# Optimization experiments

Hardware: AMD Instinct MI355X
Metric: run time of the kernel (lower is better)

The kernel has to match this reference:

```python
import jax, jax.numpy as jnp
import numpy as np

N_NODES = 50000
N_EDGES = 800000
HIDDEN = 128
HEADS = 8
HEAD_DIM = HIDDEN // HEADS
N_LAYERS = 2
BATCH = 64
INPUT = 300


def setup_inputs() -> dict:
    key = jax.random.key(0)
    ks = jax.random.split(key, 10)
    s = 0.05
    word_embed_matrix = jax.random.normal(ks[0], (N_NODES, INPUT), dtype=jnp.float32)
    edge_index = jax.random.randint(ks[1], (2, N_EDGES), 0, N_NODES, dtype=jnp.int32)
    target_idx = jax.random.randint(ks[2], (BATCH,), 0, N_NODES, dtype=jnp.int32)
    # labels: first half positive, second half negative (batch/2 pos as in original loss)
    label_id = jnp.concatenate([jnp.ones(BATCH // 2, jnp.int32), jnp.zeros(BATCH // 2, jnp.int32)])
    lin1_W = jax.random.normal(ks[3], (INPUT, HIDDEN), dtype=jnp.float32) * s
    lin1_b = jnp.zeros((HIDDEN,), jnp.float32)
    gat_W = jax.random.normal(ks[4], (N_LAYERS, HIDDEN, HIDDEN), dtype=jnp.float32) * s
    gat_att_src = jax.random.normal(ks[5], (N_LAYERS, HEADS, HEAD_DIM), dtype=jnp.float32) * s
    gat_att_dst = jax.random.normal(ks[6], (N_LAYERS, HEADS, HEAD_DIM), dtype=jnp.float32) * s
    gat_bias = jnp.zeros((N_LAYERS, HIDDEN), jnp.float32)
    lin3_W = jax.random.normal(ks[7], (HIDDEN, 1), dtype=jnp.float32) * s
    lin3_b = jnp.zeros((1,), jnp.float32)
    return {"word_embed_matrix": word_embed_matrix, "edge_index": edge_index,
            "target_idx": target_idx, "label_id": label_id,
            "lin1_W": lin1_W, "lin1_b": lin1_b, "gat_W": gat_W,
            "gat_att_src": gat_att_src, "gat_att_dst": gat_att_dst,
            "gat_bias": gat_bias, "lin3_W": lin3_W, "lin3_b": lin3_b}


def gat_layer(x, src, dst, W, a_src, a_dst, b):
    # x: [N, HIDDEN]; src/dst: [E'] (self loops included)
    N = x.shape[0]
    h = (x @ W).reshape(N, HEADS, HEAD_DIM)               # [N,H,C]
    alpha_src = jnp.sum(h * a_src, axis=-1)               # [N,H]
    alpha_dst = jnp.sum(h * a_dst, axis=-1)               # [N,H]
    e = jax.nn.leaky_relu(alpha_src[src] + alpha_dst[dst], 0.2)  # [E',H]
    # softmax over incoming edges of each dst node (segment softmax)
    emax = jax.ops.segment_max(e, dst, num_segments=N)    # [N,H]
    ee = jnp.exp(e - emax[dst])
    denom = jax.ops.segment_sum(ee, dst, num_segments=N)  # [N,H]
    alpha = ee / denom[dst]                               # [E',H]
    msg = h[src] * alpha[:, :, None]                      # [E',H,C]
    out = jax.ops.segment_sum(msg, dst, num_segments=N)   # [N,H,C]
    return out.reshape(N, HIDDEN) + b


def reference(word_embed_matrix, edge_index, target_idx, label_id,
              lin1_W, lin1_b, gat_W, gat_att_src, gat_att_dst, gat_bias,
              lin3_W, lin3_b):
    N = word_embed_matrix.shape[0]
    # add self loops (PyG GATConv default)
    loop = jnp.arange(N, dtype=edge_index.dtype)
    src = jnp.concatenate([edge_index[0], loop])
    dst = jnp.concatenate([edge_index[1], loop])
    x = word_embed_matrix @ lin1_W + lin1_b
    for i in range(N_LAYERS):
        x = jax.nn.elu(gat_layer(x, src, dst, gat_W[i], gat_att_src[i], gat_att_dst[i], gat_bias[i]))
    target_embed = x[target_idx]                          # [B, HIDDEN]
    total_score = (target_embed @ lin3_W + lin3_b)[:, 0]  # [B]
    # labels are [1]*B/2 + [0]*B/2 (static layout, matches label_id)
    half = BATCH // 2
    pos_score = total_score[:half]
    neg_score = total_score[half:]
    loss = jnp.mean(jax.nn.relu(1.0 - (pos_score - neg_score)))
    return (total_score, loss)
```

## Files before the change

kernel.cpp:

```cpp
#include <hip/hip_runtime.h>
#include <math.h>

#define N_NODES 50000
#define N_EDGESI 800000
#define E_TOT   850000
#define HIDDEN  128
#define HEADS   8
#define HEAD_DIM 16
#define INPUT   300
#define BATCH   64

#define NR    128
#define RSZ   391
#define CAP   8192
#define CHUNK 2048
#define NSB   ((E_TOT + CHUNK - 1)/CHUNK)

typedef __bf16 bf16_t;
typedef bf16_t bf16x8 __attribute__((ext_vector_type(8)));
typedef bf16_t bf16x2 __attribute__((ext_vector_type(2)));
typedef float  f32x4  __attribute__((ext_vector_type(4)));
typedef float  f32x2  __attribute__((ext_vector_type(2)));

__global__ void wa_kernel(const float* __restrict__ W, const float* __restrict__ as,
                          const float* __restrict__ ad, float* __restrict__ Wa){
    int k = threadIdx.x;
    #pragma unroll
    for (int j = 0; j < 8; j++){
        float s1 = 0.f, s2 = 0.f;
        #pragma unroll
        for (int d = 0; d < 16; d++){
            float wv = W[k*128 + j*16 + d];
            s1 += wv * as[j*16 + d];
            s2 += wv * ad[j*16 + d];
        }
        Wa[k*16 + j]     = s1;
        Wa[k*16 + 8 + j] = s2;
    }
}

template<int K_REAL, int K_PAD, int NCOL>
__global__ void fused_pack_kernel(const float* __restrict__ W1, const float* __restrict__ Wg,
                                  const float* __restrict__ Wa, const float* __restrict__ b1,
                                  bf16_t* __restrict__ bF, float* __restrict__ bcomb){
    int idx = blockIdx.x*256 + threadIdx.x;
    if (idx < NCOL){
        float s = 0.f;
        for (int d = 0; d < 128; d++)
            s += b1[d] * ((idx < 128) ? Wg[d*128 + idx] : Wa[d*16 + (idx - 128)]);
        bcomb[idx] = s;
    }
    if (idx >= K_PAD*NCOL) return;
    int k = idx / NCOL, col = idx % NCOL;
    float v = 0.f;
    if (k < K_REAL){
        const float* w1r = W1 + k*128;
        if (col < 128){
            for (int m = 0; m < 128; m++) v += w1r[m] * Wg[m*128 + col];
        } else {
            int jj = col - 128;
            for (int m = 0; m < 128; m++) v += w1r[m] * Wa[m*16 + jj];
        }
    }
    int o = ((k >> 3)*NCOL + col)*8 + (k & 7);
    bF[o] = (bf16_t)v;
}

template<int K_REAL, int K_PAD, int NCOL, bool ALPHA>
__global__ void pack_b_kernel(const float* __restrict__ B128, const float* __restrict__ as,
                              const float* __restrict__ ad, bf16_t* __restrict__ bHi){
    int idx = blockIdx.x*256 + threadIdx.x;
    if (idx >= K_PAD*NCOL) return;
    int k = idx / NCOL, col = idx % NCOL;
    float v = 0.f;
    if (k < K_REAL){
        if (!ALPHA || col < 128){
            v = B128[k*128 + col];
        } else {
            int jj = col - 128;
            const float* a = (jj < 8) ? (as + jj*16) : (ad + (jj-8)*16);
            const float* wrow = B128 + k*128 + (jj & 7)*16;
            float s = 0.f;
            #pragma unroll
            for (int d = 0; d < 16; d++) s += wrow[d]*a[d];
            v = s;
        }
    }
    int o = ((k >> 3)*NCOL + col)*8 + (k & 7);
    bHi[o] = (bf16_t)v;
}

template<int K_REAL, int K_PAD, int NT, int GH, int PD, bool A_BF16, bool BIAS_EPI, bool ALPHA, bool OUT8>
__global__ __launch_bounds__(256)
void mfma_gemm6_kernel(const void* __restrict__ A_, const bf16_t* __restrict__ bHi,
                       const float* __restrict__ bias, void* __restrict__ outP,
                       float* __restrict__ asrc_out, float* __restrict__ adst_out, int M)
{
    constexpr int NCOL   = NT * 16;
    constexpr int KSTEPS = K_PAD / 32;
    constexpr int KSPP   = GH / 4;
    constexpr int NPASS  = KSTEPS / KSPP;
    constexpr int PELEM  = GH * NCOL * 8;
    constexpr int SIT    = PELEM / 2048;
    static_assert(KSPP * NPASS == KSTEPS && SIT * 2048 == PELEM, "");
    __shared__ bf16_t blds[PELEM];

    int tid = threadIdx.x, lane = tid & 63, w = tid >> 6;
    int l15 = lane & 15, lg = lane >> 4;
    int m0 = (blockIdx.x*4 + w) * 16;
    int mrow = m0 + l15; if (mrow >= M) mrow = M - 1;

    const float*  arowF = (const float*) A_ + (size_t)mrow*K_REAL;
    const bf16_t* arowB = (const bf16_t*)A_ + (size_t)mrow*K_REAL;

    float4 pva[PD], pvb[PD];
    bf16x8 pab[PD];
    #pragma unroll
    for (int i = 0; i < PD; i++){
        int k0 = i*32 + lg*8;
        if (A_BF16){
            pab[i] = *(const bf16x8*)&arowB[k0];
        } else {
            pva[i] = (k0 + 3 < K_REAL) ? *(const float4*)&arowF[k0]     : (float4){0.f,0.f,0.f,0.f};
            pvb[i] = (k0 + 7 < K_REAL) ? *(const float4*)&arowF[k0 + 4] : (float4){0.f,0.f,0.f,0.f};
        }
    }

    f32x4 acc[NT];
    #pragma unroll
    for (int c = 0; c < NT; c++) acc[c] = (f32x4){0.f,0.f,0.f,0.f};

    #pragma unroll
    for (int p = 0; p < NPASS; p++){
        const bf16_t* gB = bHi + (size_t)p*PELEM;
        if (p) __syncthreads();
        #pragma unroll
        for (int it = 0; it < SIT; it++){
            int idx = (tid + it*256)*8;
            *(bf16x8*)&blds[idx] = *(const bf16x8*)&gB[idx];
        }
        __syncthreads();

        #pragma unroll
        for (int i = 0; i < KSPP; i++){
            const int ks = p*KSPP + i;
            const int sl = ks % PD;
            bf16x8 ah;
            if (A_BF16){
                ah = pab[sl];
            } else {
                float4 va = pva[sl], vb = pvb[sl];
                float f[8] = {va.x, va.y, va.z, va.w, vb.x, vb.y, vb.z, vb.w};
                #pragma unroll
                for (int q = 0; q < 8; q++) ah[q] = (bf16_t)f[q];
            }
            if (ks + PD < KSTEPS){
                int k0 = (ks + PD)*32 + lg*8;
                if (A_BF16){
                    pab[sl] = *(const bf16x8*)&arowB[k0];
                } else {
                    pva[sl] = (k0 + 3 < K_REAL) ? *(const float4*)&arowF[k0]     : (float4){0.f,0.f,0.f,0.f};
                    pvb[sl] = (k0 + 7 < K_REAL) ? *(const float4*)&arowF[k0 + 4] : (float4){0.f,0.f,0.f,0.f};
                }
            }
            int gloc = i*4 + lg;
            const bf16_t* b_base = &blds[(gloc*NCOL + l15)*8];
            #pragma unroll
            for (int c = 0; c < NT; c++){
                bf16x8 bh = *(const bf16x8*)&b_base[c*128];
                acc[c] = __builtin_amdgcn_mfma_f32_16x16x32_bf16(ah, bh, acc[c], 0,0,0);
            }
        }
    }

    #pragma unroll
    for (int c = 0; c < 8; c++){
        int col = c*16 + l15;
        float bv = BIAS_EPI ? bias[col] : 0.f;
        #pragma unroll
        for (int r = 0; r < 4; r++){
            int m = m0 + lg*4 + r;
            if (m < M){
                float v = acc[c][r] + bv;
                if (OUT8){
                    int pk = __builtin_amdgcn_cvt_pk_fp8_f32(v, v, 0, false);
                    ((unsigned char*)outP)[(size_t)m*128 + col] = (unsigned char)(pk & 0xff);
                } else {
                    ((bf16_t*)outP)[(size_t)m*128 + col] = (bf16_t)v;
                }
            }
        }
    }
    if (ALPHA){
        float bv8 = BIAS_EPI ? bias[128 + l15] : 0.f;
        #pragma unroll
        for (int r = 0; r < 4; r++){
            int m = m0 + lg*4 + r;
            if (m < M){
                float v = acc[8][r] + bv8;
                if (l15 < 8) asrc_out[m*8 + l15]       = v;
                else         adst_out[m*8 + (l15 - 8)] = v;
            }
        }
    }
}

__global__ void zero_cnt_kernel(int* __restrict__ bucket_cnt){
    bucket_cnt[threadIdx.x] = 0;
}

__global__ __launch_bounds__(256)
void block_sort_kernel(const int* __restrict__ ei, int* __restrict__ bucket_cnt,
                       int2* __restrict__ pairs2){
    __shared__ int2 stageL[CHUNK];
    __shared__ int2 sortedL[CHUNK];
    __shared__ unsigned short binL[CHUNK];
    __shared__ int histL[NR], lstartL[NR], lcurL[NR], gofsL[NR];
    int tid = threadIdx.x, b = blockIdx.x;
    int e0 = b*CHUNK, e1 = e0 + CHUNK; if (e1 > E_TOT) e1 = E_TOT;
    int n = e1 - e0;
    if (tid < NR) histL[tid] = 0;
    __syncthreads();
    for (int i = tid; i < n; i += 256){
        int e = e0 + i;
        int s, d;
        if (e < N_EDGESI){ s = ei[e]; d = ei[N_EDGESI + e]; }
        else { s = e - N_EDGESI; d = s; }
        stageL[i] = make_int2(s, d);
        atomicAdd(&histL[d/RSZ], 1);
    }
    __syncthreads();
    if (tid < NR) lstartL[tid] = histL[tid];
    __syncthreads();
    for (int off = 1; off < NR; off <<= 1){
        int t = 0;
        if (tid < NR && tid >= off) t = lstartL[tid - off];
        __syncthreads();
        if (tid < NR) lstartL[tid] += t;
        __syncthreads();
    }
    if (tid < NR){
        int excl = lstartL[tid] - histL[tid];
        lstartL[tid] = excl;
        lcurL[tid]   = excl;
    }
    __syncthreads();
    for (int i = tid; i < n; i += 256){
        int2 pr = stageL[i];
        int bb = pr.y / RSZ;
        int pos = atomicAdd(&lcurL[bb], 1);
        sortedL[pos] = pr;
        binL[pos] = (unsigned short)bb;
    }
    __syncthreads();
    if (tid < NR) gofsL[tid] = atomicAdd(&bucket_cnt[tid], histL[tid]);
    __syncthreads();
    for (int i = tid; i < n; i += 256){
        int bb = binL[i];
        int dst = bb*CAP + gofsL[bb] + (i - lstartL[bb]);
        pairs2[dst] = sortedL[i];
    }
}

__global__ void rbase_scan_kernel(const int* __restrict__ bucket_cnt, int* __restrict__ rbase){
    __shared__ int s[NR];
    int t = threadIdx.x;
    s[t] = bucket_cnt[t];
    __syncthreads();
    for (int off = 1; off < NR; off <<= 1){
        int u = (t >= off) ? s[t - off] : 0;
        __syncthreads();
        s[t] += u;
        __syncthreads();
    }
    rbase[t + 1] = s[t];
    if (t == 0) rbase[0] = 0;
}

__global__ __launch_bounds__(512)
void csr_finalize_kernel(const int2* __restrict__ pairs2, const int* __restrict__ bucket_cnt,
                         const int* __restrict__ rbase, int* __restrict__ col_src,
                         int* __restrict__ row_ptr){
    __shared__ int2 pairsL[CAP];
    __shared__ int  colL[CAP];
    __shared__ int  degL[512];
    __shared__ int  startL[512];
    __shared__ int  curL[512];
    int tid = threadIdx.x, r = blockIdx.x;
    int cnt = bucket_cnt[r], base = rbase[r];
    degL[tid] = 0;
    __syncthreads();
    for (int i = tid; i < cnt; i += 512){
        int2 pr = pairs2[r*CAP + i];
        pairsL[i] = pr;
        atomicAdd(&degL[pr.y - r*RSZ], 1);
    }
    __syncthreads();
    int v = degL[tid];
    for (int off = 1; off < 512; off <<= 1){
        int u = (tid >= off) ? degL[tid - off] : 0;
        __syncthreads();
        degL[tid] += u;
        __syncthreads();
    }
    int excl = degL[tid] - v;
    startL[tid] = excl;
    curL[tid]   = excl;
    __syncthreads();
    for (int i = tid; i < cnt; i += 512){
        int2 pr = pairsL[i];
        int pos = atomicAdd(&curL[pr.y - r*RSZ], 1);
        colL[pos] = pr.x;
    }
    __syncthreads();
    for (int i = tid; i < cnt; i += 512)
        col_src[base + i] = colL[i];
    if (tid < RSZ){
        int node = r*RSZ + tid;
        if (node < N_NODES) row_ptr[node] = base + startL[tid];
    }
    if (r == NR-1 && tid == 0) row_ptr[N_NODES] = E_TOT;
}

__global__ __launch_bounds__(256)
void gat_aggregate_kernel(const int* __restrict__ row_ptr, const int* __restrict__ col_src,
                          const unsigned char* __restrict__ H8, const float* __restrict__ a_s,
                          const float* __restrict__ a_d, const float* __restrict__ bias,
                          bf16_t* __restrict__ xout, const int* __restrict__ nlist, int nn){
    __shared__ float alds[4][8][65];
    int wave = threadIdx.x >> 6;
    int lane = threadIdx.x & 63;
    int gid = blockIdx.x*4 + wave;
    if (gid >= nn) return;
    int d = nlist ? nlist[gid] : gid;
    int start = row_ptr[d], end = row_ptr[d + 1];
    int deg = end - start;
    int hme = lane >> 3, seg = lane & 7;

    float ad_[8];
    {
        float4 t0 = *(const float4*)&a_d[d*8];
        float4 t1 = *(const float4*)&a_d[d*8 + 4];
        ad_[0]=t0.x; ad_[1]=t0.y; ad_[2]=t0.z; ad_[3]=t0.w;
        ad_[4]=t1.x; ad_[5]=t1.y; ad_[6]=t1.z; ad_[7]=t1.w;
    }

    float acc0 = 0.f, acc1 = 0.f, dh;
    unsigned hoff = 2u*lane;

    if (deg <= 64){
        bool act = lane < deg;
        int sreg = 0;
        float e[8];
        #pragma unroll
        for (int h = 0; h < 8; h++) e[h] = 0.f;
        if (act){
            sreg = col_src[start + lane];
            float4 s0 = *(const float4*)&a_s[sreg*8];
            float4 s1 = *(const float4*)&a_s[sreg*8 + 4];
            float as_[8] = {s0.x,s0.y,s0.z,s0.w,s1.x,s1.y,s1.z,s1.w};
            #pragma unroll
            for (int h = 0; h < 8; h++){
                float v = as_[h] + ad_[h];
                v = v > 0.f ? v : 0.2f*v;
                e[h] = __expf(fminf(v, 70.f));
            }
        }
        unsigned rbase = (unsigned)sreg * 128u;
        #pragma unroll
        for (int h = 0; h < 8; h++) alds[wave][h][lane] = e[h];

        const float* row = &alds[wave][hme][0];
        float s = 0.f;
        #pragma unroll
        for (int j = 0; j < 8; j++) s += row[seg*8 + j];
        s += __shfl_xor(s, 1); s += __shfl_xor(s, 2); s += __shfl_xor(s, 4);
        dh = 1.0f / s;

        float acc0b = 0.f, acc1b = 0.f;
        int iters = (deg + 7) >> 3;
        for (int it = 0; it < iters; it++){
            int p = it*8;
            unsigned o0 = __shfl(rbase, p+0) + hoff, o1 = __shfl(rbase, p+1) + hoff;
            unsigned o2 = __shfl(rbase, p+2) + hoff, o3 = __shfl(rbase, p+3) + hoff;
            unsigned o4 = __shfl(rbase, p+4) + hoff, o5 = __shfl(rbase, p+5) + hoff;
            unsigned o6 = __shfl(rbase, p+6) + hoff, o7 = __shfl(rbase, p+7) + hoff;
            unsigned short g0 = *(const unsigned short*)&H8[o0];
            unsigned short g1 = *(const unsigned short*)&H8[o1];
            unsigned short g2 = *(const unsigned short*)&H8[o2];
            unsigned short g3 = *(const unsigned short*)&H8[o3];
            unsigned short g4 = *(const unsigned short*)&H8[o4];
            unsigned short g5 = *(const unsigned short*)&H8[o5];
            unsigned short g6 = *(const unsigned short*)&H8[o6];
            unsigned short g7 = *(const unsigned short*)&H8[o7];
            float a0 = row[p+0], a1 = row[p+1], a2 = row[p+2], a3 = row[p+3];
            float a4 = row[p+4], a5 = row[p+5], a6 = row[p+6], a7 = row[p+7];
            f32x2 f0 = __builtin_amdgcn_cvt_pk_f32_fp8((int)g0, false);
            f32x2 f1 = __builtin_amdgcn_cvt_pk_f32_fp8((int)g1, false);
            f32x2 f2 = __builtin_amdgcn_cvt_pk_f32_fp8((int)g2, false);
            f32x2 f3 = __builtin_amdgcn_cvt_pk_f32_fp8((int)g3, false);
            f32x2 f4 = __builtin_amdgcn_cvt_pk_f32_fp8((int)g4, false);
            f32x2 f5 = __builtin_amdgcn_cvt_pk_f32_fp8((int)g5, false);
            f32x2 f6 = __builtin_amdgcn_cvt_pk_f32_fp8((int)g6, false);
            f32x2 f7 = __builtin_amdgcn_cvt_pk_f32_fp8((int)g7, false);
            acc0  += f0.x*a0 + f2.x*a2;
            acc1  += f0.y*a0 + f2.y*a2;
            acc0b += f1.x*a1 + f3.x*a3;
            acc1b += f1.y*a1 + f3.y*a3;
            acc0  += f4.x*a4 + f6.x*a6;
            acc1  += f4.y*a4 + f6.y*a6;
            acc0b += f5.x*a5 + f7.x*a7;
            acc1b += f5.y*a5 + f7.y*a7;
        }
        acc0 += acc0b;
        acc1 += acc1b;
    } else {
        float adh = ad_[hme];
        float s = 0.f;
        for (int p = start + seg; p < end; p += 8){
            int sn = col_src[p];
            float v = a_s[sn*8 + hme] + adh;
            v = v > 0.f ? v : 0.2f*v;
            s += __expf(fminf(v, 70.f));
        }
        s += __shfl_xor(s, 1); s += __shfl_xor(s, 2); s += __shfl_xor(s, 4);
        dh = 1.0f / s;
        for (int p = start; p < end; p++){
            int sn = col_src[p];
            float v = a_s[sn*8 + hme] + adh;
            v = v > 0.f ? v : 0.2f*v;
            float a = __expf(fminf(v, 70.f));
            unsigned short g = *(const unsigned short*)&H8[(size_t)sn*128 + hoff];
            f32x2 f = __builtin_amdgcn_cvt_pk_f32_fp8((int)g, false);
            acc0 += f.x*a;
            acc1 += f.y*a;
        }
    }

    float o0 = acc0*dh + bias[2*lane];
    float o1 = acc1*dh + bias[2*lane + 1];
    o0 = o0 > 0.f ? o0 : expm1f(o0);
    o1 = o1 > 0.f ? o1 : expm1f(o1);
    bf16x2 o = {(bf16_t)o0, (bf16_t)o1};
    *(bf16x2*)&xout[(size_t)d*HIDDEN + 2*lane] = o;
}

__global__ void head_kernel(const bf16_t* __restrict__ x, const int* __restrict__ tgt,
                            const float* __restrict__ w, const float* __restrict__ b,
                            float* __restrict__ dout){
    int t = threadIdx.x;
    const bf16_t* row = x + (size_t)tgt[t]*HIDDEN;
    float v = 0.f;
    #pragma unroll
    for (int c = 0; c < HIDDEN; c += 8){
        bf16x8 xv = *(const bf16x8*)&row[c];
        #pragma unroll
        for (int j = 0; j < 8; j++) v += (float)xv[j] * w[c + j];
    }
    float sc = v + b[0];
    dout[t] = sc;
    float neg = __shfl(sc, t + 32);
    float dlt = 1.0f - (sc - neg);
    float term = (t < 32) ? (dlt > 0.f ? dlt : 0.f) : 0.f;
    #pragma unroll
    for (int m = 32; m >= 1; m >>= 1) term += __shfl_xor(term, m);
    if (t == 0) dout[BATCH] = term * (1.0f/32.0f);
}

extern "C" void kernel_launch(void* const* d_in, const int* in_sizes, int n_in,
                              void* d_out, int out_size, void* d_ws, size_t ws_size,
                              hipStream_t stream) {
    const float* word   = (const float*)d_in[0];
    const int*   ei     = (const int*)  d_in[1];
    const int*   tgt    = (const int*)  d_in[2];
    const float* lin1W  = (const float*)d_in[4];
    const float* lin1b  = (const float*)d_in[5];
    const float* gatW   = (const float*)d_in[6];
    const float* attS   = (const float*)d_in[7];
    const float* attD   = (const float*)d_in[8];
    const float* gatB   = (const float*)d_in[9];
    const float* lin3W  = (const float*)d_in[10];
    const float* lin3b  = (const float*)d_in[11];

    char* ws = (char*)d_ws;
    size_t off = 0;
    bf16_t*        Xb       = (bf16_t*)(ws + off);        off += (size_t)N_NODES*HIDDEN*2;
    unsigned char* H8       = (unsigned char*)(ws + off); off += (size_t)N_NODES*HIDDEN;
    off = (off + 15) & ~(size_t)15;
    float*   a_s       = (float*)(ws + off);   off += (size_t)N_NODES*HEADS*4;
    float*   a_d       = (float*)(ws + off);   off += (size_t)N_NODES*HEADS*4;
    int*     row_ptr   = (int*)(ws + off);     off += (size_t)(N_NODES + 16)*4;
    int*     col_src   = (int*)(ws + off);     off += (size_t)E_TOT*4;
    int*     bucket_cnt= (int*)(ws + off);     off += 512;
    int*     rbase     = (int*)(ws + off);     off += 1024;
    int2*    pairs2    = (int2*)(ws + off);    off += (size_t)NR*CAP*8;
    bf16_t*  bF        = (bf16_t*)(ws + off);  off += (size_t)384*144*2;
    float*   Wa0       = (float*)(ws + off);   off += 128*16*4;
    float*   bcomb     = (float*)(ws + off);   off += 256;
    bf16_t*  b2        = (bf16_t*)(ws + off);  off += (size_t)128*144*2;

    const int GB = ((N_NODES + 15)/16 + 3)/4;

    zero_cnt_kernel    <<<1, NR, 0, stream>>>(bucket_cnt);
    block_sort_kernel  <<<NSB, 256, 0, stream>>>(ei, bucket_cnt, pairs2);
    rbase_scan_kernel  <<<1, NR, 0, stream>>>(bucket_cnt, rbase);
    csr_finalize_kernel<<<NR, 512, 0, stream>>>(pairs2, bucket_cnt, rbase, col_src, row_ptr);

    const float* Wg0 = gatW;
    wa_kernel<<<1, 128, 0, stream>>>(Wg0, attS, attD, Wa0);
    fused_pack_kernel<INPUT, 384, 144><<<(384*144 + 255)/256, 256, 0, stream>>>(
        lin1W, Wg0, Wa0, lin1b, bF, bcomb);
    mfma_gemm6_kernel<INPUT, 384, 9, 16, 5, false, true, true, true><<<GB, 256, 0, stream>>>(
        word, bF, bcomb, H8, a_s, a_d, N_NODES);
    gat_aggregate_kernel<<<(N_NODES + 3)/4, 256, 0, stream>>>(
        row_ptr, col_src, H8, a_s, a_d, gatB, Xb, nullptr, N_NODES);

    {
        const float* W = gatW + (size_t)HIDDEN*HIDDEN;
        pack_b_kernel<HIDDEN, 128, 144, true><<<(128*144 + 255)/256, 256, 0, stream>>>(
            W, attS + HEADS*HEAD_DIM, attD + HEADS*HEAD_DIM, b2);
        mfma_gemm6_kernel<HIDDEN, 128, 9, 16, 4, true, false, true, true><<<GB, 256, 0, stream>>>(
            Xb, b2, nullptr, H8, a_s, a_d, N_NODES);
        gat_aggregate_kernel<<<(BATCH + 3)/4, 256, 0, stream>>>(
            row_ptr, col_src, H8, a_s, a_d, gatB + HIDDEN, Xb, tgt, BATCH);
    }

    head_kernel<<<1, 64, 0, stream>>>(Xb, tgt, lin3W, lin3b, (float*)d_out);
}
```

Before: 132.2 us.

## Restrict layer-1 aggregation and layer-2 GEMM to target receptive-field frontier

```diff
diff --git a/kernel.cpp b/kernel.cpp
--- a/kernel.cpp
+++ b/kernel.cpp
@@ -15,6 +15,7 @@
 #define CAP   8192
 #define CHUNK 2048
 #define NSB   ((E_TOT + CHUNK - 1)/CHUNK)
+#define FCAP  8192
 
 typedef __bf16 bf16_t;
 typedef bf16_t bf16x8 __attribute__((ext_vector_type(8)));
@@ -90,11 +91,12 @@
     bHi[o] = (bf16_t)v;
 }
 
-template<int K_REAL, int K_PAD, int NT, int GH, int PD, bool A_BF16, bool BIAS_EPI, bool ALPHA, bool OUT8>
+template<int K_REAL, int K_PAD, int NT, int GH, int PD, bool A_BF16, bool BIAS_EPI, bool ALPHA, bool OUT8, bool INDIRECT>
 __global__ __launch_bounds__(256)
 void mfma_gemm6_kernel(const void* __restrict__ A_, const bf16_t* __restrict__ bHi,
                        const float* __restrict__ bias, void* __restrict__ outP,
-                       float* __restrict__ asrc_out, float* __restrict__ adst_out, int M)
+                       float* __restrict__ asrc_out, float* __restrict__ adst_out, int M,
+                       const int* __restrict__ rlist, const int* __restrict__ cnt_ptr)
 {
     constexpr int NCOL   = NT * 16;
     constexpr int KSTEPS = K_PAD / 32;
@@ -105,13 +107,18 @@
     static_assert(KSPP * NPASS == KSTEPS && SIT * 2048 == PELEM, "");
     __shared__ bf16_t blds[PELEM];
 
+    int mEff = M;
+    if (INDIRECT) mEff = cnt_ptr[0];
+    if ((int)(blockIdx.x*64) >= mEff) return;
+
     int tid = threadIdx.x, lane = tid & 63, w = tid >> 6;
     int l15 = lane & 15, lg = lane >> 4;
     int m0 = (blockIdx.x*4 + w) * 16;
-    int mrow = m0 + l15; if (mrow >= M) mrow = M - 1;
-
-    const float*  arowF = (const float*) A_ + (size_t)mrow*K_REAL;
-    const bf16_t* arowB = (const bf16_t*)A_ + (size_t)mrow*K_REAL;
+    int mrow = m0 + l15; if (mrow >= mEff) mrow = mEff - 1;
+    int arow_idx = INDIRECT ? rlist[mrow] : mrow;
+
+    const float*  arowF = (const float*) A_ + (size_t)arow_idx*K_REAL;
+    const bf16_t* arowB = (const bf16_t*)A_ + (size_t)arow_idx*K_REAL;
 
     float4 pva[PD], pvb[PD];
     bf16x8 pab[PD];
@@ -180,13 +187,14 @@
         #pragma unroll
         for (int r = 0; r < 4; r++){
             int m = m0 + lg*4 + r;
-            if (m < M){
+            if (m < mEff){
+                int row = INDIRECT ? rlist[m] : m;
                 float v = acc[c][r] + bv;
                 if (OUT8){
                     int pk = __builtin_amdgcn_cvt_pk_fp8_f32(v, v, 0, false);
-                    ((unsigned char*)outP)[(size_t)m*128 + col] = (unsigned char)(pk & 0xff);
+                    ((unsigned char*)outP)[(size_t)row*128 + col] = (unsigned char)(pk & 0xff);
                 } else {
-                    ((bf16_t*)outP)[(size_t)m*128 + col] = (bf16_t)v;
+                    ((bf16_t*)outP)[(size_t)row*128 + col] = (bf16_t)v;
                 }
             }
         }
@@ -196,10 +204,11 @@
         #pragma unroll
         for (int r = 0; r < 4; r++){
             int m = m0 + lg*4 + r;
-            if (m < M){
+            if (m < mEff){
+                int row = INDIRECT ? rlist[m] : m;
                 float v = acc[8][r] + bv8;
-                if (l15 < 8) asrc_out[m*8 + l15]       = v;
-                else         adst_out[m*8 + (l15 - 8)] = v;
+                if (l15 < 8) asrc_out[row*8 + l15]       = v;
+                else         adst_out[row*8 + (l15 - 8)] = v;
             }
         }
     }
@@ -322,14 +331,44 @@
     if (r == NR-1 && tid == 0) row_ptr[N_NODES] = E_TOT;
 }
 
+__global__ void build_frontier_kernel(const int* __restrict__ tgt, const int* __restrict__ row_ptr,
+                                      const int* __restrict__ col_src, int* __restrict__ list,
+                                      int* __restrict__ fcnt){
+    __shared__ int st[64], en[64], ofs[65];
+    int t = threadIdx.x;
+    if (t < 64){ int d = tgt[t]; st[t] = row_ptr[d]; en[t] = row_ptr[d + 1]; }
+    __syncthreads();
+    if (t == 0){
+        int acc = 64;
+        for (int i = 0; i < 64; i++){
+            ofs[i] = acc;
+            int n = en[i] - st[i];
+            acc += n;
+        }
+        if (acc > FCAP) acc = FCAP;
+        ofs[64] = acc;
+        fcnt[0] = acc;
+    }
+    __syncthreads();
+    if (t < 64) list[t] = tgt[t];
+    for (int i = 0; i < 64; i++){
+        int n = en[i] - st[i];
+        int o = ofs[i];
+        for (int j = t; j < n && o + j < FCAP; j += 256)
+            list[o + j] = col_src[st[i] + j];
+    }
+}
+
 __global__ __launch_bounds__(256)
 void gat_aggregate_kernel(const int* __restrict__ row_ptr, const int* __restrict__ col_src,
                           const unsigned char* __restrict__ H8, const float* __restrict__ a_s,
                           const float* __restrict__ a_d, const float* __restrict__ bias,
-                          bf16_t* __restrict__ xout, const int* __restrict__ nlist, int nn){
+                          bf16_t* __restrict__ xout, const int* __restrict__ nlist, int nn,
+                          const int* __restrict__ nn_ptr){
     __shared__ float alds[4][8][65];
     int wave = threadIdx.x >> 6;
     int lane = threadIdx.x & 63;
+    if (nn_ptr) nn = nn_ptr[0];
     int gid = blockIdx.x*4 + wave;
     if (gid >= nn) return;
     int d = nlist ? nlist[gid] : gid;
@@ -493,6 +532,8 @@
     int*     col_src   = (int*)(ws + off);     off += (size_t)E_TOT*4;
     int*     bucket_cnt= (int*)(ws + off);     off += 512;
     int*     rbase     = (int*)(ws + off);     off += 1024;
+    int*     frontier  = (int*)(ws + off);     off += (size_t)FCAP*4;
+    int*     fcnt      = (int*)(ws + off);     off += 64;
     int2*    pairs2    = (int2*)(ws + off);    off += (size_t)NR*CAP*8;
     bf16_t*  bF        = (bf16_t*)(ws + off);  off += (size_t)384*144*2;
     float*   Wa0       = (float*)(ws + off);   off += 128*16*4;
@@ -500,29 +541,31 @@
     bf16_t*  b2        = (bf16_t*)(ws + off);  off += (size_t)128*144*2;
 
     const int GB = ((N_NODES + 15)/16 + 3)/4;
+    const int FB = FCAP/64;
 
     zero_cnt_kernel    <<<1, NR, 0, stream>>>(bucket_cnt);
     block_sort_kernel  <<<NSB, 256, 0, stream>>>(ei, bucket_cnt, pairs2);
     rbase_scan_kernel  <<<1, NR, 0, stream>>>(bucket_cnt, rbase);
     csr_finalize_kernel<<<NR, 512, 0, stream>>>(pairs2, bucket_cnt, rbase, col_src, row_ptr);
+    build_frontier_kernel<<<1, 256, 0, stream>>>(tgt, row_ptr, col_src, frontier, fcnt);
 
     const float* Wg0 = gatW;
     wa_kernel<<<1, 128, 0, stream>>>(Wg0, attS, attD, Wa0);
     fused_pack_kernel<INPUT, 384, 144><<<(384*144 + 255)/256, 256, 0, stream>>>(
         lin1W, Wg0, Wa0, lin1b, bF, bcomb);
-    mfma_gemm6_kernel<INPUT, 384, 9, 16, 5, false, true, true, true><<<GB, 256, 0, stream>>>(
-        word, bF, bcomb, H8, a_s, a_d, N_NODES);
-    gat_aggregate_kernel<<<(N_NODES + 3)/4, 256, 0, stream>>>(
-        row_ptr, col_src, H8, a_s, a_d, gatB, Xb, nullptr, N_NODES);
+    mfma_gemm6_kernel<INPUT, 384, 9, 16, 5, false, true, true, true, false><<<GB, 256, 0, stream>>>(
+        word, bF, bcomb, H8, a_s, a_d, N_NODES, nullptr, nullptr);
+    gat_aggregate_kernel<<<FCAP/4, 256, 0, stream>>>(
+        row_ptr, col_src, H8, a_s, a_d, gatB, Xb, frontier, 0, fcnt);
 
     {
         const float* W = gatW + (size_t)HIDDEN*HIDDEN;
         pack_b_kernel<HIDDEN, 128, 144, true><<<(128*144 + 255)/256, 256, 0, stream>>>(
             W, attS + HEADS*HEAD_DIM, attD + HEADS*HEAD_DIM, b2);
-        mfma_gemm6_kernel<HIDDEN, 128, 9, 16, 4, true, false, true, true><<<GB, 256, 0, stream>>>(
-            Xb, b2, nullptr, H8, a_s, a_d, N_NODES);
+        mfma_gemm6_kernel<HIDDEN, 128, 9, 16, 4, true, false, true, true, true><<<FB, 256, 0, stream>>>(
+            Xb, b2, nullptr, H8, a_s, a_d, N_NODES, frontier, fcnt);
         gat_aggregate_kernel<<<(BATCH + 3)/4, 256, 0, stream>>>(
-            row_ptr, col_src, H8, a_s, a_d, gatB + HIDDEN, Xb, tgt, BATCH);
+            row_ptr, col_src, H8, a_s, a_d, gatB + HIDDEN, Xb, tgt, BATCH, nullptr);
     }
 
     head_kernel<<<1, 64, 0, stream>>>(Xb, tgt, lin3W, lin3b, (float*)d_out);
```

After: 123.4 us (median of 2 runs). 1.07x faster.
